# Optimization experiments

Measured on AMD Instinct MI355X. Metric: run time of the kernel, lower is better.

## Reference

```python
import math
import jax
import jax.numpy as jnp
import numpy as np

B, L, C = 16, 512, 1024
N_HEAD = 8
HEAD = C // N_HEAD


def setup_inputs() -> dict:
    key = jax.random.key(0)
    k1, k2, k3, k4, k5, k6 = jax.random.split(key, 6)
    x = jax.random.normal(k1, (B, L, C), dtype=jnp.float32)
    # binary adjacency (0/1) as float, as in graph data
    adj = jax.random.randint(k2, (B, L, L), 0, 2).astype(jnp.float32)
    W_qkv = jax.random.normal(k3, (C, 3 * C), dtype=jnp.float32) * (1.0 / math.sqrt(C))
    b_qkv = jax.random.normal(k4, (3 * C,), dtype=jnp.float32) * 0.02
    W_d = jax.random.normal(k5, (1, C), dtype=jnp.float32)
    b_d = jax.random.normal(k6, (C,), dtype=jnp.float32) * 0.02
    return {"x": x, "adj": adj, "W_qkv": W_qkv, "b_qkv": b_qkv, "W_d": W_d, "b_d": b_d}


def reference(x, adj, W_qkv, b_qkv, W_d, b_d):
    # degree gating (self.degree == True)
    degree = adj.sum(-1, keepdims=True)                      # [B,L,1]
    gate = jax.nn.sigmoid(degree @ W_d + b_d)                # [B,L,C]
    x = x * gate
    # fused qkv projection, chunk into qk / res / value
    qkv = x @ W_qkv + b_qkv                                  # [B,L,3C]
    qk, res, value = jnp.split(qkv, 3, axis=-1)
    def heads(t):                                            # [B,L,C] -> [B,H,L,hd]
        return t.reshape(B, L, N_HEAD, HEAD).transpose(0, 2, 1, 3)
    qk, res, value = heads(qk), heads(res), heads(value)
    qk = jax.nn.sigmoid(qk)
    # sigmoid-kernel attention scores
    attn = jnp.einsum("bhld,bhmd->bhlm", qk, qk) / math.sqrt(HEAD)
    # adjacency masking (rel_pos_bias == True)
    attn = jnp.where(adj[:, None, :, :] == 0, 0.0, attn)
    # sum-normalization instead of softmax
    attn = attn / (attn.sum(-1, keepdims=True) + 1e-6)
    out = jnp.einsum("bhlm,bhmd->bhld", attn, value) + res   # residual from qkv chunk
    out = out.transpose(0, 2, 1, 3).reshape(B, L, C)
    return jax.nn.relu(out)
```

## Files before the change

kernel.cpp:

```cpp
#include <hip/hip_runtime.h>
#include <math.h>

#define BDIM 16
#define LDIM 512
#define CDIM 1024
#define NH 8
#define HD 128
#define MROWS (BDIM * LDIM)
#define N3 (3 * CDIM)

typedef unsigned short u16;
typedef unsigned long long u64;
typedef short s8v __attribute__((ext_vector_type(8)));
typedef short s4v __attribute__((ext_vector_type(4)));
typedef float f32x4 __attribute__((ext_vector_type(4)));

__device__ __forceinline__ float sigmoidf_(float z) {
    return 1.0f / (1.0f + __expf(-z));
}
__device__ __forceinline__ u16 f2bf(float f) {
    union { float f; unsigned int u; } v; v.f = f;
    unsigned int u = v.u;
    unsigned int r = (u + 0x7FFFu + ((u >> 16) & 1u)) >> 16;
    return (u16)r;
}
__device__ __forceinline__ float bf2f(u16 b) {
    union { unsigned int u; float f; } v; v.u = ((unsigned int)b) << 16;
    return v.f;
}

__global__ __launch_bounds__(256) void prep_kernel(const float* __restrict__ adj,
                                                   const float* __restrict__ x,
                                                   const float* __restrict__ Wd,
                                                   const float* __restrict__ bd,
                                                   const float* __restrict__ W,
                                                   u64* __restrict__ adjbits,
                                                   u16* __restrict__ xg,
                                                   u16* __restrict__ Wt) {
    __shared__ float tile[64][65];
    int bid = blockIdx.x;
    int t = threadIdx.x;
    if (bid < MROWS) {
        int row = bid;
        int lane = t & 63, w = t >> 6;
        const float* a = adj + (size_t)row * LDIM;
        float s = 0.f;
        #pragma unroll
        for (int j = 0; j < 2; ++j) {
            int mc = j * 256 + w * 64;
            float v = a[mc + lane];
            s += v;
            u64 m = __ballot(v != 0.f);
            if (lane == 0) adjbits[(size_t)row * (LDIM / 64) + (mc >> 6)] = m;
        }
        #pragma unroll
        for (int off = 32; off > 0; off >>= 1) s += __shfl_down(s, off);
        if (lane == 0) tile[0][w] = s;
        __syncthreads();
        float d = tile[0][0] + tile[0][1] + tile[0][2] + tile[0][3];
        float4 xv = ((const float4*)(x + (size_t)row * CDIM))[t];
        float4 wv = ((const float4*)Wd)[t];
        float4 bv = ((const float4*)bd)[t];
        s4v o;
        o.x = (short)f2bf(xv.x * sigmoidf_(d * wv.x + bv.x));
        o.y = (short)f2bf(xv.y * sigmoidf_(d * wv.y + bv.y));
        o.z = (short)f2bf(xv.z * sigmoidf_(d * wv.z + bv.z));
        o.w = (short)f2bf(xv.w * sigmoidf_(d * wv.w + bv.w));
        ((s4v*)(xg + (size_t)row * CDIM))[t] = o;
    } else {
        int pb = bid - MROWS;
        int k0 = (pb & 15) * 64, n0 = (pb >> 4) * 64;
        int tx = t & 63, ty = t >> 6;
        #pragma unroll
        for (int yy = ty; yy < 64; yy += 4)
            tile[yy][tx] = W[(size_t)(k0 + yy) * N3 + n0 + tx];
        __syncthreads();
        #pragma unroll
        for (int yy = ty; yy < 64; yy += 4)
            Wt[(size_t)(n0 + yy) * CDIM + k0 + tx] = f2bf(tile[tx][yy]);
    }
}

__global__ __launch_bounds__(256, 4) void gemm_bf16_kernel(const u16* __restrict__ A,
                                                           const u16* __restrict__ Bt,
                                                           const float* __restrict__ bias,
                                                           u16* __restrict__ ksig,
                                                           u16* __restrict__ resb,
                                                           u16* __restrict__ vt) {
    __shared__ __align__(16) u16 smem[128 * 128];
#define BOFF (128 * 64)
    int t = threadIdx.x;
    int m0 = blockIdx.y * 128, n0 = blockIdx.x * 128;
    int lane = t & 63, w = t >> 6;
    int i15 = lane & 15, quad = lane >> 4;
    int wm = w >> 1, wn = w & 1;

    f32x4 acc[4][4];
    #pragma unroll
    for (int i = 0; i < 4; ++i)
        #pragma unroll
        for (int j = 0; j < 4; ++j) acc[i][j] = (f32x4)(0.f);

    for (int k0 = 0; k0 < CDIM; k0 += 64) {
        #pragma unroll
        for (int p = 0; p < 4; ++p) {
            int sb = (w * 4 + p) * 64;
            int s = sb + lane;
            int row = s >> 3;
            int seg = (s & 7) ^ (row & 7);
            const u16* ga = A + (size_t)(m0 + row) * CDIM + k0 + seg * 8;
            const u16* gb = Bt + (size_t)(n0 + row) * CDIM + k0 + seg * 8;
            __builtin_amdgcn_global_load_lds(
                (const __attribute__((address_space(1))) unsigned int*)ga,
                (__attribute__((address_space(3))) unsigned int*)&smem[sb * 8], 16, 0, 0);
            __builtin_amdgcn_global_load_lds(
                (const __attribute__((address_space(1))) unsigned int*)gb,
                (__attribute__((address_space(3))) unsigned int*)&smem[BOFF + sb * 8], 16, 0, 0);
        }
        __syncthreads();
        #pragma unroll
        for (int kc = 0; kc < 2; ++kc) {
            s8v aF[4], bF[4];
            #pragma unroll
            for (int mt = 0; mt < 4; ++mt) {
                int row = wm * 64 + mt * 16 + i15;
                int slot = row * 8 + ((kc * 4 + quad) ^ (i15 & 7));
                aF[mt] = *(const s8v*)&smem[slot * 8];
            }
            #pragma unroll
            for (int nt = 0; nt < 4; ++nt) {
                int row = wn * 64 + nt * 16 + i15;
                int slot = row * 8 + ((kc * 4 + quad) ^ (i15 & 7));
                bF[nt] = *(const s8v*)&smem[BOFF + slot * 8];
            }
            #pragma unroll
            for (int mt = 0; mt < 4; ++mt)
                #pragma unroll
                for (int nt = 0; nt < 4; ++nt)
                    acc[mt][nt] = __builtin_amdgcn_mfma_f32_16x16x32_bf16(aF[mt], bF[nt], acc[mt][nt], 0, 0, 0);
        }
        __syncthreads();
    }

    int chunk = n0 >> 10;
    #pragma unroll
    for (int nt = 0; nt < 4; ++nt) {
        int lcol = wn * 64 + nt * 16 + i15;
        float bv = bias[n0 + lcol];
        #pragma unroll
        for (int mt = 0; mt < 4; ++mt) {
            int lrow0 = wm * 64 + mt * 16 + quad * 4;
            #pragma unroll
            for (int r = 0; r < 4; ++r) {
                int lrow = lrow0 + r;
                float v = acc[mt][nt][r] + bv;
                if (chunk == 0) v = sigmoidf_(v);
                u16 bf = f2bf(v);
                if (chunk == 2)
                    smem[lcol * 128 + (lrow ^ ((lcol & 7) << 4))] = bf;
                else
                    smem[lrow * 128 + (lcol ^ ((lrow & 7) << 4))] = bf;
            }
        }
    }
    __syncthreads();
    if (chunk == 0) {
        int h = (n0 >> 7) & 7;
        int bb = m0 >> 9, lb = m0 & 511;
        #pragma unroll
        for (int i = 0; i < 8; ++i) {
            int idx = i * 2048 + t * 8;
            int row = idx >> 7, pc = idx & 127;
            int col = pc ^ ((row & 7) << 4);
            *(s8v*)&ksig[(((size_t)bb * NH + h) * LDIM + lb + row) * HD + col] =
                *(const s8v*)&smem[idx];
        }
    } else if (chunk == 1) {
        int c0 = n0 - CDIM;
        #pragma unroll
        for (int i = 0; i < 8; ++i) {
            int idx = i * 2048 + t * 8;
            int row = idx >> 7, pc = idx & 127;
            int col = pc ^ ((row & 7) << 4);
            *(s8v*)&resb[(size_t)(m0 + row) * CDIM + c0 + col] = *(const s8v*)&smem[idx];
        }
    } else {
        int h = (n0 - 2048) >> 7;
        int bb = m0 >> 9, lb = m0 & 511;
        #pragma unroll
        for (int i = 0; i < 8; ++i) {
            int idx = i * 2048 + t * 8;
            int d = idx >> 7, pr = idx & 127;
            int row = pr ^ ((d & 7) << 4);
            *(s8v*)&vt[(((size_t)bb * NH + h) * HD + d) * LDIM + lb + row] =
                *(const s8v*)&smem[idx];
        }
    }
#undef BOFF
}

__global__ __launch_bounds__(256) void attn_kernel(const u16* __restrict__ ksig,
                                                   const u16* __restrict__ vt,
                                                   const u16* __restrict__ resb,
                                                   const u64* __restrict__ adjbits,
                                                   float* __restrict__ out) {
    __shared__ __align__(16) u16 lds_ks[64 * 128];
    __shared__ __align__(16) u16 lds_vt[128 * 64];
    __shared__ __align__(16) u16 lds_ps[4][16][64];

    int t = threadIdx.x;
    int lane = t & 63, w = t >> 6;
    int i15 = lane & 15, quad = lane >> 4;
    int bid = blockIdx.x;
    int l0 = (bid >> 7) * 64;
    int b  = (bid >> 3) & 15;
    int h  = bid & 7;

    const u16* ksig_bh = ksig + ((size_t)b * NH + h) * LDIM * HD;
    const u16* vt_bh   = vt + ((size_t)b * NH + h) * HD * LDIM;
    const u64* abits   = adjbits + ((size_t)b * LDIM + l0 + w * 16 + quad * 4) * (LDIM / 64);

    s8v aQ[4];
    {
        const u16* qrow = ksig_bh + (size_t)(l0 + w * 16 + i15) * HD + quad * 8;
        #pragma unroll
        for (int kc = 0; kc < 4; ++kc) aQ[kc] = *(const s8v*)(qrow + kc * 32);
    }

    f32x4 accO[8];
    #pragma unroll
    for (int i = 0; i < 8; ++i) accO[i] = (f32x4)(0.f);
    float prs[4] = {0.f, 0.f, 0.f, 0.f};

    const float scale = 0.08838834764831845f;

    for (int m0 = 0; m0 < LDIM; m0 += 64) {
        #pragma unroll
        for (int p = 0; p < 4; ++p) {
            int sb = (w * 4 + p) * 64;
            int s = sb + lane;
            int row = s >> 4;
            int seg = (s & 15) ^ (row & 15);
            const u16* g = ksig_bh + (size_t)(m0 + row) * HD + seg * 8;
            __builtin_amdgcn_global_load_lds(
                (const __attribute__((address_space(1))) unsigned int*)g,
                (__attribute__((address_space(3))) unsigned int*)&lds_ks[sb * 8], 16, 0, 0);
        }
        #pragma unroll
        for (int p = 0; p < 4; ++p) {
            int sb = (w * 4 + p) * 64;
            int s = sb + lane;
            int row = s >> 3;
            int seg = (s & 7) ^ (row & 7);
            const u16* g = vt_bh + (size_t)row * LDIM + m0 + seg * 8;
            __builtin_amdgcn_global_load_lds(
                (const __attribute__((address_space(1))) unsigned int*)g,
                (__attribute__((address_space(3))) unsigned int*)&lds_vt[sb * 8], 16, 0, 0);
        }
        unsigned int mw0[4], mw1[4];
        #pragma unroll
        for (int r = 0; r < 4; ++r) {
            u64 wrd = abits[(size_t)r * (LDIM / 64) + (m0 >> 6)];
            mw0[r] = (unsigned int)wrd;
            mw1[r] = (unsigned int)(wrd >> 32);
        }
        __syncthreads();

        f32x4 S[4];
        #pragma unroll
        for (int nt = 0; nt < 4; ++nt) {
            S[nt] = (f32x4)(0.f);
            #pragma unroll
            for (int kc = 0; kc < 4; ++kc) {
                int row = nt * 16 + i15;
                int slot = row * 16 + ((kc * 4 + quad) ^ (row & 15));
                s8v bK = *(const s8v*)&lds_ks[slot * 8];
                S[nt] = __builtin_amdgcn_mfma_f32_16x16x32_bf16(aQ[kc], bK, S[nt], 0, 0, 0);
            }
        }

        #pragma unroll
        for (int nt = 0; nt < 4; ++nt) {
            int sh = (nt & 1) * 16 + i15;
            int pcol = (nt * 16 + i15) ^ (quad << 4);
            #pragma unroll
            for (int r = 0; r < 4; ++r) {
                unsigned int half = (nt < 2) ? mw0[r] : mw1[r];
                float p = ((half >> sh) & 1u) ? S[nt][r] * scale : 0.f;
                prs[r] += p;
                lds_ps[w][quad * 4 + r][pcol] = f2bf(p);
            }
        }

        {
            s8v aP[2];
            #pragma unroll
            for (int ks = 0; ks < 2; ++ks)
                aP[ks] = *(const s8v*)&lds_ps[w][i15][(ks * 32 + quad * 8) ^ ((i15 >> 2) << 4)];
            #pragma unroll
            for (int ntd = 0; ntd < 8; ++ntd) {
                #pragma unroll
                for (int ks = 0; ks < 2; ++ks) {
                    int row = ntd * 16 + i15;
                    int slot = row * 8 + ((ks * 4 + quad) ^ (row & 7));
                    s8v bV = *(const s8v*)&lds_vt[slot * 8];
                    accO[ntd] = __builtin_amdgcn_mfma_f32_16x16x32_bf16(aP[ks], bV, accO[ntd], 0, 0, 0);
                }
            }
        }
        __syncthreads();
    }

    float inv[4];
    #pragma unroll
    for (int r = 0; r < 4; ++r) {
        float s = prs[r];
        s += __shfl_xor(s, 1);
        s += __shfl_xor(s, 2);
        s += __shfl_xor(s, 4);
        s += __shfl_xor(s, 8);
        inv[r] = 1.0f / (s + 1e-6f);
    }
    #pragma unroll
    for (int ntd = 0; ntd < 8; ++ntd) {
        int dcol = h * HD + ntd * 16 + i15;
        #pragma unroll
        for (int r = 0; r < 4; ++r) {
            size_t idx = ((size_t)b * LDIM + l0 + w * 16 + quad * 4 + r) * CDIM + dcol;
            float v = accO[ntd][r] * inv[r] + bf2f(resb[idx]);
            out[idx] = fmaxf(v, 0.f);
        }
    }
}

extern "C" void kernel_launch(void* const* d_in, const int* in_sizes, int n_in,
                              void* d_out, int out_size, void* d_ws, size_t ws_size,
                              hipStream_t stream) {
    (void)in_sizes; (void)n_in; (void)out_size; (void)ws_size;
    const float* x     = (const float*)d_in[0];
    const float* adj   = (const float*)d_in[1];
    const float* W_qkv = (const float*)d_in[2];
    const float* b_qkv = (const float*)d_in[3];
    const float* W_d   = (const float*)d_in[4];
    const float* b_d   = (const float*)d_in[5];
    float* out = (float*)d_out;

    char* ws = (char*)d_ws;
    size_t off = 0;
    u64* adjb   = (u64*)(ws + off);   off += (size_t)MROWS * 8 * 8;
    u16*   xg   = (u16*)(ws + off);   off += (size_t)MROWS * CDIM * 2;
    u16*   Wt   = (u16*)(ws + off);   off += (size_t)N3 * CDIM * 2;
    u16*   ksig = (u16*)(ws + off);   off += (size_t)MROWS * CDIM * 2;
    u16*   resb = (u16*)(ws + off);   off += (size_t)MROWS * CDIM * 2;
    u16*   vt   = (u16*)(ws + off);   off += (size_t)MROWS * CDIM * 2;

    prep_kernel<<<MROWS + (CDIM / 64) * (N3 / 64), 256, 0, stream>>>(
        adj, x, W_d, b_d, W_qkv, adjb, xg, Wt);
    gemm_bf16_kernel<<<dim3(N3 / 128, MROWS / 128), 256, 0, stream>>>(xg, Wt, b_qkv, ksig, resb, vt);
    attn_kernel<<<LDIM / 64 * NH * BDIM, 256, 0, stream>>>(ksig, vt, resb, adjb, out);
}
```

Baseline: 213.8 us.

## Process two query tiles per attention block to reuse staged K/V tiles

Each attention workgroup now handles two 64-row query tiles (l0 and l0+256) and processes each staged K/V LDS tile twice, once per tile. This halves the grid and the global-to-LDS traffic for K and V per query row. In exchange, register pressure roughly doubles (two accumulator sets), which may lower occupancy, and with half as many blocks there is less parallelism to spread across the GPU.

```diff
diff --git a/kernel.cpp b/kernel.cpp
--- a/kernel.cpp
+++ b/kernel.cpp
@@ -212,25 +212,32 @@
     int lane = t & 63, w = t >> 6;
     int i15 = lane & 15, quad = lane >> 4;
     int bid = blockIdx.x;
-    int l0 = (bid >> 7) * 64;
+    int l0a = (bid >> 7) * 64;
+    int l0b = l0a + 256;
     int b  = (bid >> 3) & 15;
     int h  = bid & 7;
 
     const u16* ksig_bh = ksig + ((size_t)b * NH + h) * LDIM * HD;
     const u16* vt_bh   = vt + ((size_t)b * NH + h) * HD * LDIM;
-    const u64* abits   = adjbits + ((size_t)b * LDIM + l0 + w * 16 + quad * 4) * (LDIM / 64);
-
-    s8v aQ[4];
+    const u64* abA = adjbits + ((size_t)b * LDIM + l0a + w * 16 + quad * 4) * (LDIM / 64);
+    const u64* abB = adjbits + ((size_t)b * LDIM + l0b + w * 16 + quad * 4) * (LDIM / 64);
+
+    s8v aQa[4], aQb[4];
     {
-        const u16* qrow = ksig_bh + (size_t)(l0 + w * 16 + i15) * HD + quad * 8;
-        #pragma unroll
-        for (int kc = 0; kc < 4; ++kc) aQ[kc] = *(const s8v*)(qrow + kc * 32);
-    }
-
-    f32x4 accO[8];
+        const u16* qA = ksig_bh + (size_t)(l0a + w * 16 + i15) * HD + quad * 8;
+        const u16* qB = ksig_bh + (size_t)(l0b + w * 16 + i15) * HD + quad * 8;
+        #pragma unroll
+        for (int kc = 0; kc < 4; ++kc) {
+            aQa[kc] = *(const s8v*)(qA + kc * 32);
+            aQb[kc] = *(const s8v*)(qB + kc * 32);
+        }
+    }
+
+    f32x4 accA[8], accB[8];
     #pragma unroll
-    for (int i = 0; i < 8; ++i) accO[i] = (f32x4)(0.f);
-    float prs[4] = {0.f, 0.f, 0.f, 0.f};
+    for (int i = 0; i < 8; ++i) { accA[i] = (f32x4)(0.f); accB[i] = (f32x4)(0.f); }
+    float prsA[4] = {0.f, 0.f, 0.f, 0.f};
+    float prsB[4] = {0.f, 0.f, 0.f, 0.f};
 
     const float scale = 0.08838834764831845f;
 
@@ -257,42 +264,41 @@
                 (const __attribute__((address_space(1))) unsigned int*)g,
                 (__attribute__((address_space(3))) unsigned int*)&lds_vt[sb * 8], 16, 0, 0);
         }
-        unsigned int mw0[4], mw1[4];
+        unsigned int mwA0[4], mwA1[4], mwB0[4], mwB1[4];
         #pragma unroll
         for (int r = 0; r < 4; ++r) {
-            u64 wrd = abits[(size_t)r * (LDIM / 64) + (m0 >> 6)];
-            mw0[r] = (unsigned int)wrd;
-            mw1[r] = (unsigned int)(wrd >> 32);
-        }
-        __syncthreads();
-
-        f32x4 S[4];
-        #pragma unroll
-        for (int nt = 0; nt < 4; ++nt) {
-            S[nt] = (f32x4)(0.f);
-            #pragma unroll
-            for (int kc = 0; kc < 4; ++kc) {
-                int row = nt * 16 + i15;
-                int slot = row * 16 + ((kc * 4 + quad) ^ (row & 15));
-                s8v bK = *(const s8v*)&lds_ks[slot * 8];
-                S[nt] = __builtin_amdgcn_mfma_f32_16x16x32_bf16(aQ[kc], bK, S[nt], 0, 0, 0);
-            }
-        }
-
-        #pragma unroll
-        for (int nt = 0; nt < 4; ++nt) {
-            int sh = (nt & 1) * 16 + i15;
-            int pcol = (nt * 16 + i15) ^ (quad << 4);
-            #pragma unroll
-            for (int r = 0; r < 4; ++r) {
-                unsigned int half = (nt < 2) ? mw0[r] : mw1[r];
-                float p = ((half >> sh) & 1u) ? S[nt][r] * scale : 0.f;
-                prs[r] += p;
-                lds_ps[w][quad * 4 + r][pcol] = f2bf(p);
-            }
-        }
+            u64 wa = abA[(size_t)r * (LDIM / 64) + (m0 >> 6)];
+            u64 wb = abB[(size_t)r * (LDIM / 64) + (m0 >> 6)];
+            mwA0[r] = (unsigned int)wa; mwA1[r] = (unsigned int)(wa >> 32);
+            mwB0[r] = (unsigned int)wb; mwB1[r] = (unsigned int)(wb >> 32);
+        }
+        __syncthreads();
 
         {
+            f32x4 S[4];
+            #pragma unroll
+            for (int nt = 0; nt < 4; ++nt) {
+                S[nt] = (f32x4)(0.f);
+                #pragma unroll
+                for (int kc = 0; kc < 4; ++kc) {
+                    int row = nt * 16 + i15;
+                    int slot = row * 16 + ((kc * 4 + quad) ^ (row & 15));
+                    s8v bK = *(const s8v*)&lds_ks[slot * 8];
+                    S[nt] = __builtin_amdgcn_mfma_f32_16x16x32_bf16(aQa[kc], bK, S[nt], 0, 0, 0);
+                }
+            }
+            #pragma unroll
+            for (int nt = 0; nt < 4; ++nt) {
+                int sh = (nt & 1) * 16 + i15;
+                int pcol = (nt * 16 + i15) ^ (quad << 4);
+                #pragma unroll
+                for (int r = 0; r < 4; ++r) {
+                    unsigned int half = (nt < 2) ? mwA0[r] : mwA1[r];
+                    float p = ((half >> sh) & 1u) ? S[nt][r] * scale : 0.f;
+                    prsA[r] += p;
+                    lds_ps[w][quad * 4 + r][pcol] = f2bf(p);
+                }
+            }
             s8v aP[2];
             #pragma unroll
             for (int ks = 0; ks < 2; ++ks)
@@ -304,31 +310,76 @@
                     int row = ntd * 16 + i15;
                     int slot = row * 8 + ((ks * 4 + quad) ^ (row & 7));
                     s8v bV = *(const s8v*)&lds_vt[slot * 8];
-                    accO[ntd] = __builtin_amdgcn_mfma_f32_16x16x32_bf16(aP[ks], bV, accO[ntd], 0, 0, 0);
-                }
-            }
-        }
-        __syncthreads();
-    }
-
-    float inv[4];
+                    accA[ntd] = __builtin_amdgcn_mfma_f32_16x16x32_bf16(aP[ks], bV, accA[ntd], 0, 0, 0);
+                }
+            }
+        }
+        {
+            f32x4 S[4];
+            #pragma unroll
+            for (int nt = 0; nt < 4; ++nt) {
+                S[nt] = (f32x4)(0.f);
+                #pragma unroll
+                for (int kc = 0; kc < 4; ++kc) {
+                    int row = nt * 16 + i15;
+                    int slot = row * 16 + ((kc * 4 + quad) ^ (row & 15));
+                    s8v bK = *(const s8v*)&lds_ks[slot * 8];
+                    S[nt] = __builtin_amdgcn_mfma_f32_16x16x32_bf16(aQb[kc], bK, S[nt], 0, 0, 0);
+                }
+            }
+            #pragma unroll
+            for (int nt = 0; nt < 4; ++nt) {
+                int sh = (nt & 1) * 16 + i15;
+                int pcol = (nt * 16 + i15) ^ (quad << 4);
+                #pragma unroll
+                for (int r = 0; r < 4; ++r) {
+                    unsigned int half = (nt < 2) ? mwB0[r] : mwB1[r];
+                    float p = ((half >> sh) & 1u) ? S[nt][r] * scale : 0.f;
+                    prsB[r] += p;
+                    lds_ps[w][quad * 4 + r][pcol] = f2bf(p);
+                }
+            }
+            s8v aP[2];
+            #pragma unroll
+            for (int ks = 0; ks < 2; ++ks)
+                aP[ks] = *(const s8v*)&lds_ps[w][i15][(ks * 32 + quad * 8) ^ ((i15 >> 2) << 4)];
+            #pragma unroll
+            for (int ntd = 0; ntd < 8; ++ntd) {
+                #pragma unroll
+                for (int ks = 0; ks < 2; ++ks) {
+                    int row = ntd * 16 + i15;
+                    int slot = row * 8 + ((ks * 4 + quad) ^ (row & 7));
+                    s8v bV = *(const s8v*)&lds_vt[slot * 8];
+                    accB[ntd] = __builtin_amdgcn_mfma_f32_16x16x32_bf16(aP[ks], bV, accB[ntd], 0, 0, 0);
+                }
+            }
+        }
+        __syncthreads();
+    }
+
+    float invA[4], invB[4];
     #pragma unroll
     for (int r = 0; r < 4; ++r) {
-        float s = prs[r];
-        s += __shfl_xor(s, 1);
-        s += __shfl_xor(s, 2);
-        s += __shfl_xor(s, 4);
-        s += __shfl_xor(s, 8);
-        inv[r] = 1.0f / (s + 1e-6f);
+        float sa = prsA[r];
+        sa += __shfl_xor(sa, 1); sa += __shfl_xor(sa, 2);
+        sa += __shfl_xor(sa, 4); sa += __shfl_xor(sa, 8);
+        invA[r] = 1.0f / (sa + 1e-6f);
+        float sb = prsB[r];
+        sb += __shfl_xor(sb, 1); sb += __shfl_xor(sb, 2);
+        sb += __shfl_xor(sb, 4); sb += __shfl_xor(sb, 8);
+        invB[r] = 1.0f / (sb + 1e-6f);
     }
     #pragma unroll
     for (int ntd = 0; ntd < 8; ++ntd) {
         int dcol = h * HD + ntd * 16 + i15;
         #pragma unroll
         for (int r = 0; r < 4; ++r) {
-            size_t idx = ((size_t)b * LDIM + l0 + w * 16 + quad * 4 + r) * CDIM + dcol;
-            float v = accO[ntd][r] * inv[r] + bf2f(resb[idx]);
-            out[idx] = fmaxf(v, 0.f);
+            size_t idxA = ((size_t)b * LDIM + l0a + w * 16 + quad * 4 + r) * CDIM + dcol;
+            float va = accA[ntd][r] * invA[r] + bf2f(resb[idxA]);
+            out[idxA] = fmaxf(va, 0.f);
+            size_t idxB = ((size_t)b * LDIM + l0b + w * 16 + quad * 4 + r) * CDIM + dcol;
+            float vb = accB[ntd][r] * invB[r] + bf2f(resb[idxB]);
+            out[idxB] = fmaxf(vb, 0.f);
         }
     }
 }
@@ -357,5 +408,5 @@
     prep_kernel<<<MROWS + (CDIM / 64) * (N3 / 64), 256, 0, stream>>>(
         adj, x, W_d, b_d, W_qkv, adjb, xg, Wt);
     gemm_bf16_kernel<<<dim3(N3 / 128, MROWS / 128), 256, 0, stream>>>(xg, Wt, b_qkv, ksig, resb, vt);
-    attn_kernel<<<LDIM / 64 * NH * BDIM, 256, 0, stream>>>(ksig, vt, resb, adjb, out);
-}
+    attn_kernel<<<LDIM / 128 * NH * BDIM, 256, 0, stream>>>(ksig, vt, resb, adjb, out);
+}
```

Result: no change. 210.5 us (-1.6%).
